# Kernel tuning notes

Measured on AMD Instinct MI355X. Metric: run time of the kernel, lower is better.

## Reference

```python
import jax, jax.numpy as jnp
import numpy as np

KH, KW = 3, 3      # kernel_size
FILTERS = 32
MINVAL, MAXVAL = -0.45, -0.15


def setup_inputs() -> dict:
    key = jax.random.key(0)
    k1, k2 = jax.random.split(key)
    x = jax.random.normal(k1, (16, 256, 256, 1), dtype=jnp.float32)
    # dilation_weights: (1, 1, 1, kh*kw, filters), RandomUniform(minval, maxval)
    w = jax.random.uniform(k2, (1, 1, 1, KH * KW, FILTERS),
                           minval=MINVAL, maxval=MAXVAL, dtype=jnp.float32)
    return {"x": x, "w": w}


def reference(x, w):
    # x: (B, H, W, 1) channels_last; w: (1, 1, 1, kh*kw, filters)
    B, H, W, _ = x.shape
    Ho, Wo = H - KH + 1, W - KW + 1  # VALID padding, stride 1
    # extract_patches equivalent: (B, Ho, Wo, kh*kw), row-major over window
    patches = jnp.stack(
        [x[:, i:i + Ho, j:j + Wo, 0] for i in range(KH) for j in range(KW)],
        axis=-1,
    )
    # broadcast-add structuring element, max-reduce over patch dim (tropical conv)
    return jnp.max(patches[..., None] + w, axis=3)  # (B, Ho, Wo, filters)
```

## Files before the change

### kernel.cpp

```cpp
#include <hip/hip_runtime.h>


#define BB 16
#define HH 256
#define WW 256
#define FF 32
#define HO 254
#define WO 254
#define RPT 4

__device__ __forceinline__ float4 f4add(float a, float4 w) {
    return make_float4(a + w.x, a + w.y, a + w.z, a + w.w);
}
__device__ __forceinline__ float4 f4max(float4 a, float4 b) {
    return make_float4(fmaxf(a.x, b.x), fmaxf(a.y, b.y),
                       fmaxf(a.z, b.z), fmaxf(a.w, b.w));
}

__global__ __launch_bounds__(256) void
dilate_kernel(const float* __restrict__ x, const float* __restrict__ w,
              float* __restrict__ out) {
    const int fq = threadIdx.x & 7;
    const int pp = threadIdx.x >> 3;
    const int j0 = (blockIdx.x << 7) + (pp << 2);
    const int i0 = blockIdx.y * RPT;
    const int b  = blockIdx.z;

    const float4* __restrict__ w4 = (const float4*)w + fq;
    float4 wv[9];
#pragma unroll
    for (int p = 0; p < 9; ++p) wv[p] = w4[p * 8];

    const bool tail_ok = (j0 + 5 < WW);
    float xv[RPT + 2][6];
#pragma unroll
    for (int r = 0; r < RPT + 2; ++r) {
        int row = i0 + r;
        row = (row < HH) ? row : (HH - 1);
        const float* xb = x + ((b * HH + row) * WW + j0);
        const float4 lo = *(const float4*)xb;
        xv[r][0] = lo.x; xv[r][1] = lo.y; xv[r][2] = lo.z; xv[r][3] = lo.w;
        if (tail_ok) {
            const float2 hi = *(const float2*)(xb + 4);
            xv[r][4] = hi.x; xv[r][5] = hi.y;
        } else {
            xv[r][4] = 0.f; xv[r][5] = 0.f;
        }
    }

#pragma unroll
    for (int rr = 0; rr < RPT; ++rr) {
        const int i = i0 + rr;
        if (i < HO) {
            float4* o4 = (float4*)out + (((b * HO + i) * WO + j0) * 8 + fq);
#pragma unroll
            for (int k = 0; k < 4; ++k) {
                float4 t0, t1, t2;
#pragma unroll
                for (int r = 0; r < 3; ++r) {
                    float4 s0 = f4add(xv[rr + r][k + 0], wv[r * 3 + 0]);
                    float4 s1 = f4add(xv[rr + r][k + 1], wv[r * 3 + 1]);
                    float4 s2 = f4add(xv[rr + r][k + 2], wv[r * 3 + 2]);
                    float4 t  = f4max(f4max(s0, s1), s2);
                    if (r == 0) t0 = t; else if (r == 1) t1 = t; else t2 = t;
                }
                const float4 m = f4max(f4max(t0, t1), t2);

                if (j0 + k < WO) o4[k * 8] = m;
            }
        }
    }
}

extern "C" void kernel_launch(void* const* d_in, const int* in_sizes, int n_in,
                              void* d_out, int out_size, void* d_ws, size_t ws_size,
                              hipStream_t stream) {
    const float* x = (const float*)d_in[0];
    const float* w = (const float*)d_in[1];
    float* out = (float*)d_out;

    dim3 grid((WO + 127) / 128, (HO + RPT - 1) / RPT, BB);
    dilate_kernel<<<grid, 256, 0, stream>>>(x, w, out);
}
```

Before: 139.1 us.

## Loop each block over full row width with strided pixel assignment

Each block now covers the whole output width, looping 8 times over 32-pixel strips, instead of two blocks each handling 128 columns. Each thread processes one pixel per iteration, so consecutive threads write contiguous output and stores coalesce better than with the 4-pixel-per-thread layout. The cost is half as many blocks, more loop overhead, and scalar overlapping input loads instead of vector loads.

Measured after the change: 146.6 us. +5.3%, slower.

```diff
diff --git a/kernel.cpp b/kernel.cpp
--- a/kernel.cpp
+++ b/kernel.cpp
@@ -21,8 +21,7 @@
 dilate_kernel(const float* __restrict__ x, const float* __restrict__ w,
               float* __restrict__ out) {
     const int fq = threadIdx.x & 7;
-    const int pp = threadIdx.x >> 3;
-    const int j0 = (blockIdx.x << 7) + (pp << 2);
+    const int px = threadIdx.x >> 3;
     const int i0 = blockIdx.y * RPT;
     const int b  = blockIdx.z;
 
@@ -31,42 +30,44 @@
 #pragma unroll
     for (int p = 0; p < 9; ++p) wv[p] = w4[p * 8];
 
-    const bool tail_ok = (j0 + 5 < WW);
-    float xv[RPT + 2][6];
+    const float* __restrict__ xb = x + (size_t)b * HH * WW;
+    const float* xr[RPT + 2];
 #pragma unroll
     for (int r = 0; r < RPT + 2; ++r) {
         int row = i0 + r;
         row = (row < HH) ? row : (HH - 1);
-        const float* xb = x + ((b * HH + row) * WW + j0);
-        const float4 lo = *(const float4*)xb;
-        xv[r][0] = lo.x; xv[r][1] = lo.y; xv[r][2] = lo.z; xv[r][3] = lo.w;
-        if (tail_ok) {
-            const float2 hi = *(const float2*)(xb + 4);
-            xv[r][4] = hi.x; xv[r][5] = hi.y;
-        } else {
-            xv[r][4] = 0.f; xv[r][5] = 0.f;
-        }
+        xr[r] = xb + row * WW;
     }
 
+#pragma unroll 2
+    for (int it = 0; it < 8; ++it) {
+        const int j  = it * 32 + px;
+        const int jl = (j < WO) ? j : (WO - 1);
+
+        float xv[RPT + 2][3];
 #pragma unroll
-    for (int rr = 0; rr < RPT; ++rr) {
-        const int i = i0 + rr;
-        if (i < HO) {
-            float4* o4 = (float4*)out + (((b * HO + i) * WO + j0) * 8 + fq);
+        for (int r = 0; r < RPT + 2; ++r) {
+            xv[r][0] = xr[r][jl + 0];
+            xv[r][1] = xr[r][jl + 1];
+            xv[r][2] = xr[r][jl + 2];
+        }
+
 #pragma unroll
-            for (int k = 0; k < 4; ++k) {
-                float4 t0, t1, t2;
+        for (int rr = 0; rr < RPT; ++rr) {
+            const int i = i0 + rr;
+            float4 t0, t1, t2;
 #pragma unroll
-                for (int r = 0; r < 3; ++r) {
-                    float4 s0 = f4add(xv[rr + r][k + 0], wv[r * 3 + 0]);
-                    float4 s1 = f4add(xv[rr + r][k + 1], wv[r * 3 + 1]);
-                    float4 s2 = f4add(xv[rr + r][k + 2], wv[r * 3 + 2]);
-                    float4 t  = f4max(f4max(s0, s1), s2);
-                    if (r == 0) t0 = t; else if (r == 1) t1 = t; else t2 = t;
-                }
-                const float4 m = f4max(f4max(t0, t1), t2);
+            for (int r = 0; r < 3; ++r) {
+                float4 s0 = f4add(xv[rr + r][0], wv[r * 3 + 0]);
+                float4 s1 = f4add(xv[rr + r][1], wv[r * 3 + 1]);
+                float4 s2 = f4add(xv[rr + r][2], wv[r * 3 + 2]);
+                float4 t  = f4max(f4max(s0, s1), s2);
+                if (r == 0) t0 = t; else if (r == 1) t1 = t; else t2 = t;
+            }
+            const float4 m = f4max(f4max(t0, t1), t2);
 
-                if (j0 + k < WO) o4[k * 8] = m;
+            if (j < WO && i < HO) {
+                *((float4*)out + (((size_t)(b * HO + i) * WO + j) * 8 + fq)) = m;
             }
         }
     }
@@ -79,6 +80,6 @@
     const float* w = (const float*)d_in[1];
     float* out = (float*)d_out;
 
-    dim3 grid((WO + 127) / 128, (HO + RPT - 1) / RPT, BB);
+    dim3 grid(1, (HO + RPT - 1) / RPT, BB);
     dilate_kernel<<<grid, 256, 0, stream>>>(x, w, out);
 }
```
